# Kernel optimization log

Hardware: AMD Instinct MI355X
Metric: run time of the kernel (lower is better)

The kernel has to match this reference:

```python
import jax, jax.numpy as jnp
import numpy as np

S, V, H = 32, 16, 8            # hidden_scalars, hidden_vectors, num_heads
N, E = 10000, 100000           # nodes, edges
NRB, RH = 16, 64               # radial basis, radial MLP hidden
TH = S + 3 * V                 # packed irreps width (80)
WNUM = S * S + V * S + S * V + 2 * V * V  # TP weight_numel = 2560


def setup_inputs() -> dict:
    key = jax.random.key(0)
    ks = jax.random.split(key, 16)
    inp = {}
    inp["node_features"] = jax.random.normal(ks[0], (N, TH), jnp.float32)
    inp["edge_index"] = jax.random.randint(ks[1], (2, E), 0, N)
    inp["edge_sh"] = jax.random.normal(ks[2], (E, 4), jnp.float32)
    inp["edge_radial"] = jax.random.uniform(ks[3], (E, NRB), dtype=jnp.float32)
    inp["edge_envelope"] = jax.random.uniform(ks[4], (E,), dtype=jnp.float32)
    # radial MLP
    inp["W1"] = jax.random.normal(ks[5], (NRB, RH), jnp.float32) / np.sqrt(NRB)
    inp["b1"] = jnp.zeros((RH,), jnp.float32)
    inp["W2"] = jax.random.normal(ks[6], (RH, WNUM), jnp.float32) / np.sqrt(RH)
    inp["b2"] = jnp.zeros((WNUM,), jnp.float32)
    # attention query/key nets (scalar channels only)
    inp["Wq"] = jax.random.normal(ks[7], (S, H), jnp.float32) / np.sqrt(S)
    inp["bq"] = jnp.zeros((H,), jnp.float32)
    inp["Wk"] = jax.random.normal(ks[8], (S, H), jnp.float32) / np.sqrt(S)
    inp["bk"] = jnp.zeros((H,), jnp.float32)
    # equivariant linears (per-irrep channel mixing, e3nn style, no bias)
    inp["Wout_s"] = jax.random.normal(ks[9], (S, S), jnp.float32)
    inp["Wout_v"] = jax.random.normal(ks[10], (V, V), jnp.float32)
    inp["Wg_s"] = jax.random.normal(ks[11], (S, S + V), jnp.float32)
    inp["Wg_v"] = jax.random.normal(ks[12], (V, V), jnp.float32)
    # equivariant batch norm params
    inp["bn_ws"] = jnp.ones((S,), jnp.float32)
    inp["bn_bs"] = jnp.zeros((S,), jnp.float32)
    inp["bn_wv"] = jnp.ones((V,), jnp.float32)
    return inp


def _forward(node_features, edge_sh, edge_radial, edge_envelope,
             W1, b1, W2, b2, Wq, bq, Wk, bk,
             Wout_s, Wout_v, Wg_s, Wg_v, bn_ws, bn_bs, bn_wv, src, dst):
    # --- per-edge TP weights from radial MLP -> (E, WNUM), the big tensor ---
    tp_w = jax.nn.silu(edge_radial @ W1 + b1) @ W2 + b2
    offs = np.cumsum([0, S * S, V * S, S * V, V * V, V * V])
    WA = tp_w[:, offs[0]:offs[1]].reshape(-1, S, S)  # 0e x 0e -> 0e
    WB = tp_w[:, offs[1]:offs[2]].reshape(-1, V, S)  # 1o x 1o -> 0e
    WC = tp_w[:, offs[2]:offs[3]].reshape(-1, S, V)  # 0e x 1o -> 1o
    WD = tp_w[:, offs[3]:offs[4]].reshape(-1, V, V)  # 1o x 0e -> 1o
    WE = tp_w[:, offs[4]:offs[5]].reshape(-1, V, V)  # 1o x 1o -> 1o (cross)

    # --- gather source features, split irreps ---
    s_src = node_features[src, :S]                       # (E, S)
    v_src = node_features[src, S:].reshape(-1, V, 3)     # (E, V, 3)
    y0 = edge_sh[:, 0:1]                                 # (E, 1) l=0
    y1 = edge_sh[:, 1:4]                                 # (E, 3) l=1

    a0 = 1.0 / np.sqrt(S + V)       # path normalization, 0e output
    a1 = 1.0 / np.sqrt(S + 2 * V)   # path normalization, 1o output

    dot = (v_src * y1[:, None, :]).sum(-1) / np.sqrt(3.0)          # (E, V)
    msg_s = a0 * (jnp.einsum('es,esk->ek', s_src * y0, WA)
                  + jnp.einsum('ev,evk->ek', dot, WB))             # (E, S)
    crs = jnp.cross(v_src, y1[:, None, :]) / np.sqrt(2.0)          # (E, V, 3)
    msg_v = a1 * (jnp.einsum('es,ec,esk->ekc', s_src, y1, WC)
                  + jnp.einsum('evc,evk->ekc', v_src * y0[:, :, None], WD)
                  + jnp.einsum('evc,evk->ekc', crs, WE))           # (E, V, 3)
    messages = jnp.concatenate([msg_s, msg_v.reshape(-1, 3 * V)], axis=-1)

    # --- scatter-softmax attention over incoming edges per destination ---
    q = node_features[dst, :S] @ Wq + bq                 # (E, H)
    k = msg_s @ Wk + bk                                  # (E, H)
    logits = (q * k).sum(-1) / np.sqrt(H) + jnp.log(edge_envelope + 1e-8)
    mx = jax.ops.segment_max(logits, dst, num_segments=N)
    ex = jnp.exp(logits - mx[dst])
    den = jax.ops.segment_sum(ex, dst, num_segments=N)
    attn = ex / (den[dst] + 1e-8)                        # (E,)

    agg = jax.ops.segment_sum(attn[:, None] * messages, dst, num_segments=N)

    # --- equivariant output linear ---
    agg_s = agg[:, :S] @ Wout_s / np.sqrt(S)
    agg_v = jnp.einsum('nvc,vw->nwc', agg[:, S:].reshape(-1, V, 3), Wout_v) / np.sqrt(V)

    # --- gate ---
    gs = agg_s @ Wg_s / np.sqrt(S)                       # (N, S+V)
    gv = jnp.einsum('nvc,vw->nwc', agg_v, Wg_v) / np.sqrt(V)
    s = jax.nn.silu(gs[:, :S])
    g = jax.nn.sigmoid(gs[:, S:])
    v = g[:, :, None] * gv
    act = jnp.concatenate([s, v.reshape(-1, 3 * V)], axis=-1)

    # --- residual + equivariant batch norm ---
    x = act + node_features
    xs = x[:, :S]
    xv = x[:, S:].reshape(-1, V, 3)
    mean = xs.mean(0)
    var = xs.var(0)
    xs = (xs - mean) / jnp.sqrt(var + 1e-5) * bn_ws + bn_bs
    vn = (xv * xv).mean(-1).mean(0)                      # (V,) component norm
    xv = xv * (bn_wv / jnp.sqrt(vn + 1e-5))[None, :, None]
    return jnp.concatenate([xs, xv.reshape(-1, 3 * V)], axis=-1)


def reference(node_features, edge_index, edge_sh, edge_radial, edge_envelope,
              W1, b1, W2, b2, Wq, bq, Wk, bk,
              Wout_s, Wout_v, Wg_s, Wg_v, bn_ws, bn_bs, bn_wv):
    src, dst = edge_index[0], edge_index[1]
    return _forward(node_features, edge_sh, edge_radial, edge_envelope,
                    W1, b1, W2, b2, Wq, bq, Wk, bk,
                    Wout_s, Wout_v, Wg_s, Wg_v, bn_ws, bn_bs, bn_wv, src, dst)
```

## Files before the change

kernel.cpp:

```cpp
#include <hip/hip_runtime.h>
#include <math.h>

typedef __bf16 bf16x8 __attribute__((ext_vector_type(8)));
typedef __bf16 bf16x4 __attribute__((ext_vector_type(4)));
typedef float  f32x4  __attribute__((ext_vector_type(4)));
typedef float  f32x2  __attribute__((ext_vector_type(2)));
typedef unsigned long long u64x2 __attribute__((ext_vector_type(2)));

__device__ __forceinline__ float silu_f(float x){ return x / (1.f + __expf(-x)); }
__device__ __forceinline__ float sigm_f(float x){ return 1.f / (1.f + __expf(-x)); }

__device__ __forceinline__ float ntld_f(const float* p){
  return __builtin_nontemporal_load(p);
}
__device__ __forceinline__ float ntbf(const __bf16* p){
  unsigned short us = __builtin_nontemporal_load((const unsigned short*)p);
  union { unsigned u; float f; } cv; cv.u = ((unsigned)us) << 16;
  return cv.f;
}
__device__ __forceinline__ void nt_store_f(float* p, float v){
  __builtin_nontemporal_store(v, p);
}
__device__ __forceinline__ void nt_store_b8(__bf16* p, bf16x8 v){
  u64x2 u; __builtin_memcpy(&u, &v, 16);
  __builtin_nontemporal_store(u, (u64x2*)p);
}
__device__ __forceinline__ f32x2 b4lo(bf16x4 v){ f32x2 r; r[0]=(float)v[0]; r[1]=(float)v[1]; return r; }
__device__ __forceinline__ f32x2 b4hi(bf16x4 v){ f32x2 r; r[0]=(float)v[2]; r[1]=(float)v[3]; return r; }

__global__ void __launch_bounds__(256) k_setup(const float* __restrict__ W2,
    __bf16* __restrict__ W2t, const int* __restrict__ ei, int* __restrict__ cnt,
    const float* __restrict__ nf, const float* __restrict__ Wq,
    const float* __restrict__ bq, const float* __restrict__ Wk,
    const float* __restrict__ bk, float* __restrict__ kvt, float* __restrict__ carr,
    int nbPrep, int nbHist, int N, int E){
  int b = blockIdx.x, t = threadIdx.x;
  if (b < nbPrep){
    int gid = b*256 + t;
    int h = gid / 2560;
    int col = gid - h*2560;
    W2t[(size_t)(h>>5)*81920 + col*32 + (h&31)] = (__bf16)ntld_f(&W2[gid]);
    return;
  }
  if (b < nbPrep + nbHist){
    int e = (b - nbPrep)*256 + t;
    if (e < E) atomicAdd(&cnt[ei[E+e]], 1);
    return;
  }
  __shared__ float M[32][33];
  __shared__ float mb[32];
  __shared__ float nfl[64][33];
  __shared__ float bqbk_s;
  const int n0 = (b - nbPrep - nbHist)*64;
  for (int idx = t; idx < 1024; idx += 256){
    int s = idx >> 5, i = idx & 31;
    float acc = 0.f;
    #pragma unroll
    for (int j = 0; j < 8; ++j) acc += Wq[s*8+j]*Wk[i*8+j];
    M[s][i] = acc;
  }
  if (t < 32){
    float acc = 0.f;
    #pragma unroll
    for (int j = 0; j < 8; ++j) acc += Wq[t*8+j]*bk[j];
    mb[t] = acc;
  }
  if (t == 0){
    float acc = 0.f;
    #pragma unroll
    for (int j = 0; j < 8; ++j) acc += bq[j]*bk[j];
    bqbk_s = acc;
  }
  for (int idx = t; idx < 2048; idx += 256){
    int nl = idx >> 5, s = idx & 31;
    int n = n0 + nl;
    nfl[nl][s] = (n < N) ? nf[(size_t)n*80 + s] : 0.f;
  }
  __syncthreads();
  for (int idx = t; idx < 2048; idx += 256){
    int nl = idx >> 5, i = idx & 31;
    int n = n0 + nl;
    if (n < N){
      float acc = 0.f;
      #pragma unroll 8
      for (int s = 0; s < 32; ++s) acc += nfl[nl][s]*M[s][i];
      kvt[(size_t)n*32 + i] = acc;
    }
  }
  if (t < 64){
    int n = n0 + t;
    if (n < N){
      float acc = bqbk_s;
      #pragma unroll 8
      for (int s = 0; s < 32; ++s) acc += nfl[t][s]*mb[s];
      carr[n] = acc;
    }
  }
}

__global__ void __launch_bounds__(1024) k_scan(const int* __restrict__ cnt,
    int* __restrict__ cursor, float* __restrict__ bnacc, int N, int E){
  __shared__ int part[1024];
  int t = threadIdx.x;
  if (t < 80) bnacc[t] = 0.f;
  int chunk = (N + 1023) >> 10;
  int lo = t*chunk, hi = min(lo+chunk, N);
  int s = 0;
  for (int i = lo; i < hi; ++i) s += cnt[i];
  part[t] = s;
  __syncthreads();
  for (int off = 1; off < 1024; off <<= 1){
    int v = (t >= off) ? part[t-off] : 0;
    __syncthreads();
    part[t] += v;
    __syncthreads();
  }
  int base = (t == 0) ? 0 : part[t-1];
  for (int i = lo; i < hi; ++i){
    cursor[i] = base;
    base += cnt[i];
  }
}

__global__ void __launch_bounds__(256) k_prep(
    const float* __restrict__ nf, const int* __restrict__ ei,
    const float* __restrict__ sh, const float* __restrict__ radial,
    const float* __restrict__ W1, const float* __restrict__ b1,
    int* __restrict__ cursor,
    __bf16* __restrict__ uG, __bf16* __restrict__ cabG, __bf16* __restrict__ cvG,
    int* __restrict__ permG, int E, int NT)
{
  __shared__ float featT[80][65];
  __shared__ float radl[64][17];
  __shared__ float shlT[4][64];
  __shared__ float w1l[1024];
  __shared__ float b1l[64];
  __shared__ __align__(16) __bf16 u_l[64][72];
  __shared__ __align__(16) __bf16 cab_l[48][64];
  __shared__ __align__(16) __bf16 cv_l[64][3][64];
  __shared__ int src_l[64];

  const int t = threadIdx.x;
  const int e0 = blockIdx.x*64;
  const int tg0 = blockIdx.x*4;

  if (t < 64){
    int ee = e0 + t;
    if (ee < E){
      src_l[t] = ei[ee];
      permG[ee] = atomicAdd(&cursor[ei[(size_t)E+ee]], 1);
    } else src_l[t] = ei[E-1];
    b1l[t] = b1[t];
  }
  {
    int e = t >> 2, c = t & 3;
    int ec = min(e0+e, E-1);
    shlT[c][e] = ntld_f(&sh[(size_t)ec*4+c]);
  }
  for (int i = t; i < 1024; i += 256){
    int e = i >> 4, r = i & 15;
    int ec = min(e0+e, E-1);
    radl[e][r] = ntld_f(&radial[(size_t)ec*16+r]);
  }
  *(float4*)&w1l[t*4] = ((const float4*)W1)[t];
  __syncthreads();

  for (int i = t; i < 5120; i += 256){
    int e = i / 80, idx = i - e*80;
    featT[idx][e] = nf[(size_t)src_l[e]*80 + idx];
  }
  for (int i = t; i < 4096; i += 256){
    int e = i & 63, h = i >> 6;
    float acc = b1l[h];
    #pragma unroll
    for (int r = 0; r < 16; ++r) acc += radl[e][r]*w1l[r*64+h];
    u_l[e][h] = (__bf16)silu_f(acc);
  }
  __syncthreads();

  const float inv_s3 = 0.57735026918962576f;
  const float inv_s2 = 0.70710678118654752f;
  const float a0 = 0.14433756729740643f;
  const float a1 = 0.125f;

  for (int i = t; i < 3072; i += 256){
    int r = i >> 6, e = i & 63;
    float val;
    if (r < 32) val = a0 * shlT[0][e] * featT[r][e];
    else {
      int v = r - 32;
      float dot = (featT[32+v*3][e]*shlT[1][e] + featT[33+v*3][e]*shlT[2][e]
                 + featT[34+v*3][e]*shlT[3][e]) * inv_s3;
      val = a0 * dot;
    }
    cab_l[r][e] = (__bf16)val;
  }
  for (int i = t; i < 12288; i += 256){
    int e = i & 63, r = (i >> 6) & 63, c = i >> 12;
    float val;
    if (r < 32) val = a1 * shlT[1+c][e] * featT[r][e];
    else if (r < 48){
      int v = r - 32;
      val = a1 * shlT[0][e] * featT[32+v*3+c][e];
    } else {
      int v = r - 48;
      int c1 = c+1; if (c1 > 2) c1 -= 3;
      int c2 = c+2; if (c2 > 2) c2 -= 3;
      val = a1 * inv_s2 * (featT[32+v*3+c1][e]*shlT[1+c2][e]
                         - featT[32+v*3+c2][e]*shlT[1+c1][e]);
    }
    cv_l[r][c][e] = (__bf16)val;
  }
  __syncthreads();

  for (int i = t; i < 512; i += 256){
    int tl = i >> 7, rem = i & 127, k8 = rem >> 4, e = rem & 15;
    if (tg0 + tl < NT){
      bf16x8 v = *(const bf16x8*)&u_l[tl*16 + e][k8*8];
      *(bf16x8*)((char*)uG + (size_t)(tg0+tl)*2048 + k8*256 + e*16) = v;
    }
  }
  for (int i = t; i < 384; i += 256){
    int tl = i / 96, rem = i - tl*96, r = rem >> 1, h = rem & 1;
    if (tg0 + tl < NT){
      bf16x8 v = *(const bf16x8*)&cab_l[r][tl*16 + h*8];
      *(bf16x8*)((char*)cabG + (size_t)(tg0+tl)*1536 + r*32 + h*16) = v;
    }
  }
  for (int i = t; i < 1536; i += 256){
    int tl = i / 384, rem = i - tl*384, r = rem / 6, rem2 = rem - r*6,
        c = rem2 >> 1, h = rem2 & 1;
    if (tg0 + tl < NT){
      bf16x8 v = *(const bf16x8*)&cv_l[r][c][tl*16 + h*8];
      *(bf16x8*)((char*)cvG + (size_t)(tg0+tl)*6144 + r*96 + c*32 + h*16) = v;
    }
  }
}

#define LOAD_PANEL(BASE_IT, NITS) do {                                         \
    for (int idx = t; idx < (NITS)*128; idx += 512){                           \
      int itl_ = idx >> 7, rem_ = idx & 127, half_ = rem_ >> 6, r6_ = rem_ & 63;\
      int col_ = r6_ >> 2, quad_ = r6_ & 3;                                    \
      *(float4*)(panel + itl_*2048 + half_*1024 + quad_*256 + col_*16) =       \
        *(const float4*)(w2b + half_*163840 + (size_t)((BASE_IT)+itl_)*1024    \
                         + col_*64 + quad_*16);                                \
    }                                                                          \
    for (int i = t; i < (NITS)*16; i += 512) b2l[i] = b2[(BASE_IT)*16 + i];    \
  } while(0)

#define CAB_STAGE(TGC, BASE) do {                                              \
    bf16x8 x_ = *(const bf16x8*)(cabGb + (size_t)(TGC)*1536 + lane*16);        \
    bf16x4 y_ = *(const bf16x4*)(cabGb + (size_t)(TGC)*1536 + 1024 + lane*8);  \
    *(bf16x8*)(myCab + (BASE) + lane*16) = x_;                                 \
    *(bf16x4*)(myCab + (BASE) + 1024 + lane*8) = y_;                           \
  } while(0)

#define CV_STAGE(TGC, BASE, HALF) do {                                         \
    bf16x8 c0_ = *(const bf16x8*)(cvGb + (size_t)(TGC)*6144 + (HALF)*3072 + lane*48);\
    bf16x8 c1_ = *(const bf16x8*)(cvGb + (size_t)(TGC)*6144 + (HALF)*3072 + lane*48 + 16);\
    bf16x8 c2_ = *(const bf16x8*)(cvGb + (size_t)(TGC)*6144 + (HALF)*3072 + lane*48 + 32);\
    *(bf16x8*)(myCab + (BASE) + lane*48)      = c0_;                           \
    *(bf16x8*)(myCab + (BASE) + lane*48 + 16) = c1_;                           \
    *(bf16x8*)(myCab + (BASE) + lane*48 + 32) = c2_;                           \
  } while(0)

#define S_PAIR(SECOND, CBA, CBB, TA, TB) do {                                  \
    _Pragma("unroll 4")                                                        \
    for (int itl = 0; itl < 48; ++itl){                                        \
      bf16x8 B0_ = *(const bf16x8*)(panel + itl*2048 + laneOff);               \
      bf16x8 B1_ = *(const bf16x8*)(panel + itl*2048 + 1024 + laneOff);        \
      f32x4 dA_; dA_[0]=0;dA_[1]=0;dA_[2]=0;dA_[3]=0; f32x4 dB_ = dA_;         \
      dA_ = __builtin_amdgcn_mfma_f32_16x16x32_bf16(u##TA##_0, B0_, dA_, 0,0,0);\
      dB_ = __builtin_amdgcn_mfma_f32_16x16x32_bf16(u##TB##_0, B0_, dB_, 0,0,0);\
      dA_ = __builtin_amdgcn_mfma_f32_16x16x32_bf16(u##TA##_1, B1_, dA_, 0,0,0);\
      dB_ = __builtin_amdgcn_mfma_f32_16x16x32_bf16(u##TB##_1, B1_, dB_, 0,0,0);\
      const float bias_ = b2l[itl*16 + nlo];                                   \
      f32x2 bb_; bb_[0]=bias_; bb_[1]=bias_;                                   \
      f32x2 dAlo_ = __builtin_shufflevector(dA_,dA_,0,1) + bb_;                \
      f32x2 dAhi_ = __builtin_shufflevector(dA_,dA_,2,3) + bb_;                \
      f32x2 dBlo_ = __builtin_shufflevector(dB_,dB_,0,1) + bb_;                \
      f32x2 dBhi_ = __builtin_shufflevector(dB_,dB_,2,3) + bb_;                \
      const int r_ = (SECOND)*24 + (itl>>1);                                   \
      bf16x4 cA_ = *(const bf16x4*)(myCab + (CBA) + r_*32 + quad*8);           \
      bf16x4 cB_ = *(const bf16x4*)(myCab + (CBB) + r_*32 + quad*8);           \
      if (itl & 1){                                                            \
        s1l##TA += b4lo(cA_)*dAlo_; s1h##TA += b4hi(cA_)*dAhi_;                \
        s1l##TB += b4lo(cB_)*dBlo_; s1h##TB += b4hi(cB_)*dBhi_;                \
      } else {                                                                 \
        s0l##TA += b4lo(cA_)*dAlo_; s0h##TA += b4hi(cA_)*dAhi_;                \
        s0l##TB += b4lo(cB_)*dBlo_; s0h##TB += b4hi(cB_)*dBhi_;                \
      }                                                                        \
    }                                                                          \
  } while(0)

#define V_PAIR(TA, TB) do {                                                    \
    _Pragma("unroll 4")                                                        \
    for (int itl = 0; itl < 32; ++itl){                                        \
      bf16x8 B0_ = *(const bf16x8*)(panel + itl*2048 + laneOff);               \
      bf16x8 B1_ = *(const bf16x8*)(panel + itl*2048 + 1024 + laneOff);        \
      f32x4 dA_; dA_[0]=0;dA_[1]=0;dA_[2]=0;dA_[3]=0; f32x4 dB_ = dA_;         \
      dA_ = __builtin_amdgcn_mfma_f32_16x16x32_bf16(u##TA##_0, B0_, dA_, 0,0,0);\
      dB_ = __builtin_amdgcn_mfma_f32_16x16x32_bf16(u##TB##_0, B0_, dB_, 0,0,0);\
      dA_ = __builtin_amdgcn_mfma_f32_16x16x32_bf16(u##TA##_1, B1_, dA_, 0,0,0);\
      dB_ = __builtin_amdgcn_mfma_f32_16x16x32_bf16(u##TB##_1, B1_, dB_, 0,0,0);\
      const float bias_ = b2l[itl*16 + nlo];                                   \
      f32x2 bb_; bb_[0]=bias_; bb_[1]=bias_;                                   \
      f32x2 dAlo_ = __builtin_shufflevector(dA_,dA_,0,1) + bb_;                \
      f32x2 dAhi_ = __builtin_shufflevector(dA_,dA_,2,3) + bb_;                \
      f32x2 dBlo_ = __builtin_shufflevector(dB_,dB_,0,1) + bb_;                \
      f32x2 dBhi_ = __builtin_shufflevector(dB_,dB_,2,3) + bb_;                \
      const char* cbA_ = myCab + itl*96;                                       \
      const char* cbB_ = myCab + 3072 + itl*96;                                \
      bf16x4 q0_ = *(const bf16x4*)(cbA_ + quad*8);                            \
      bf16x4 q1_ = *(const bf16x4*)(cbA_ + 32 + quad*8);                       \
      bf16x4 q2_ = *(const bf16x4*)(cbA_ + 64 + quad*8);                       \
      v0l##TA += b4lo(q0_)*dAlo_; v0h##TA += b4hi(q0_)*dAhi_;                  \
      v1l##TA += b4lo(q1_)*dAlo_; v1h##TA += b4hi(q1_)*dAhi_;                  \
      v2l##TA += b4lo(q2_)*dAlo_; v2h##TA += b4hi(q2_)*dAhi_;                  \
      q0_ = *(const bf16x4*)(cbB_ + quad*8);                                   \
      q1_ = *(const bf16x4*)(cbB_ + 32 + quad*8);                              \
      q2_ = *(const bf16x4*)(cbB_ + 64 + quad*8);                              \
      v0l##TB += b4lo(q0_)*dBlo_; v0h##TB += b4hi(q0_)*dBhi_;                  \
      v1l##TB += b4lo(q1_)*dBlo_; v1h##TB += b4hi(q1_)*dBhi_;                  \
      v2l##TB += b4lo(q2_)*dBlo_; v2h##TB += b4hi(q2_)*dBhi_;                  \
    }                                                                          \
  } while(0)

#define S_FLUSH(TG, S0LO, S0HI, S1LO, S1HI) do {                               \
      myOut[(eb+0)*56 + nlo] = S0LO[0];                                        \
      myOut[(eb+1)*56 + nlo] = S0LO[1];                                        \
      myOut[(eb+2)*56 + nlo] = S0HI[0];                                        \
      myOut[(eb+3)*56 + nlo] = S0HI[1];                                        \
      myOut[(eb+0)*56 + 16+nlo] = S1LO[0];                                     \
      myOut[(eb+1)*56 + 16+nlo] = S1LO[1];                                     \
      myOut[(eb+2)*56 + 16+nlo] = S1HI[0];                                     \
      myOut[(eb+3)*56 + 16+nlo] = S1HI[1];                                     \
      const int e0e = (TG)*16;                                                 \
      { int e = lane>>2, seg = lane&3, eg = e0e + e;                           \
        if (eg < E){                                                           \
          f32x4 m0 = *(const f32x4*)&myOut[e*56 + seg*8];                      \
          f32x4 m1 = *(const f32x4*)&myOut[e*56 + seg*8 + 4];                  \
          bf16x8 o; o[0]=(__bf16)m0[0]; o[1]=(__bf16)m0[1];                    \
          o[2]=(__bf16)m0[2]; o[3]=(__bf16)m0[3]; o[4]=(__bf16)m1[0];          \
          o[5]=(__bf16)m1[1]; o[6]=(__bf16)m1[2]; o[7]=(__bf16)m1[3];          \
          nt_store_b8(msgs + (size_t)permG[eg]*80 + seg*8, o);                 \
        } }                                                                    \
      for (int r8 = 0; r8 < 2; ++r8){                                          \
        int e = r8*8 + (lane>>3), kq = lane&7, eg = e0e + e;                   \
        f32x4 ms = *(const f32x4*)&myOut[e*56 + kq*4];                         \
        int dn = ei[(size_t)E + min(eg, E-1)];                                 \
        const float* kvp = kvt + (size_t)dn*32 + kq*4;                         \
        float part = ms[0]*kvp[0]+ms[1]*kvp[1]+ms[2]*kvp[2]+ms[3]*kvp[3];      \
        part += __shfl_xor(part, 1);                                           \
        part += __shfl_xor(part, 2);                                           \
        part += __shfl_xor(part, 4);                                           \
        if (kq == 0 && eg < E){                                                \
          float lg = (part + carr[dn]) * 0.35355339059327373f                  \
                   + logf(ntld_f(&env[eg]) + 1e-8f);                           \
          nt_store_f(&logits_s[permG[eg]], lg);                                \
        } }                                                                    \
  } while(0)

#define V_FLUSH(TG, V0LO, V0HI, V1LO, V1HI, V2LO, V2HI) do {                   \
      const int cb2 = nlo*3;                                                   \
      myOut[(eb+0)*56 + cb2+0] = V0LO[0];                                      \
      myOut[(eb+1)*56 + cb2+0] = V0LO[1];                                      \
      myOut[(eb+2)*56 + cb2+0] = V0HI[0];                                      \
      myOut[(eb+3)*56 + cb2+0] = V0HI[1];                                      \
      myOut[(eb+0)*56 + cb2+1] = V1LO[0];                                      \
      myOut[(eb+1)*56 + cb2+1] = V1LO[1];                                      \
      myOut[(eb+2)*56 + cb2+1] = V1HI[0];                                      \
      myOut[(eb+3)*56 + cb2+1] = V1HI[1];                                      \
      myOut[(eb+0)*56 + cb2+2] = V2LO[0];                                      \
      myOut[(eb+1)*56 + cb2+2] = V2LO[1];                                      \
      myOut[(eb+2)*56 + cb2+2] = V2HI[0];                                      \
      myOut[(eb+3)*56 + cb2+2] = V2HI[1];                                      \
      const int e0e = (TG)*16;                                                 \
      for (int i = lane; i < 96; i += 64){                                     \
        int e = i/6, seg = i - (i/6)*6, eg = e0e + e;                          \
        if (eg < E){                                                           \
          f32x4 m0 = *(const f32x4*)&myOut[e*56 + seg*8];                      \
          f32x4 m1 = *(const f32x4*)&myOut[e*56 + seg*8 + 4];                  \
          bf16x8 o; o[0]=(__bf16)m0[0]; o[1]=(__bf16)m0[1];                    \
          o[2]=(__bf16)m0[2]; o[3]=(__bf16)m0[3]; o[4]=(__bf16)m1[0];          \
          o[5]=(__bf16)m1[1]; o[6]=(__bf16)m1[2]; o[7]=(__bf16)m1[3];          \
          nt_store_b8(msgs + (size_t)permG[eg]*80 + 32 + seg*8, o);            \
        } }                                                                    \
  } while(0)

__global__ void __launch_bounds__(512, 1) k_edge(
    const __bf16* __restrict__ W2t, const float* __restrict__ b2,
    const __bf16* __restrict__ uG, const __bf16* __restrict__ cabG,
    const __bf16* __restrict__ cvG, const int* __restrict__ ei,
    const int* __restrict__ permG, const float* __restrict__ kvt,
    const float* __restrict__ carr, const float* __restrict__ env,
    __bf16* __restrict__ msgs, float* __restrict__ logits_s, int E, int NT)
{
  __shared__ __align__(16) char panel[98304];
  __shared__ __align__(16) char wstage[8][6144];
  __shared__ float b2l[768];

  const int t = threadIdx.x;
  const int lane = t & 63;
  const int wv   = t >> 6;
  const int quad = lane >> 4;
  const int nlo  = lane & 15;
  const int wgid = blockIdx.x*8 + wv;
  const int laneOff = quad*256 + nlo*16;
  const int uOff    = quad*256 + nlo*16;
  char*  myCab = wstage[wv];
  float* myOut = (float*)wstage[wv];
  const char* w2b   = (const char*)W2t;
  const char* uGb   = (const char*)uG;
  const char* cabGb = (const char*)cabG;
  const char* cvGb  = (const char*)cvG;

  const int tA0 = wgid, tB0 = wgid + 2048, tA1 = wgid + 4096, tB1 = wgid + 6144;
  const bool hA0 = tA0 < NT, hB0 = tB0 < NT, hA1 = tA1 < NT, hB1 = tB1 < NT;
  const int cA0 = min(tA0, NT-1), cB0 = min(tB0, NT-1);
  const int cA1 = min(tA1, NT-1), cB1 = min(tB1, NT-1);

  const bf16x8 uA0_0 = *(const bf16x8*)(uGb + (size_t)cA0*2048 + uOff);
  const bf16x8 uA0_1 = *(const bf16x8*)(uGb + (size_t)cA0*2048 + 1024 + uOff);
  const bf16x8 uB0_0 = *(const bf16x8*)(uGb + (size_t)cB0*2048 + uOff);
  const bf16x8 uB0_1 = *(const bf16x8*)(uGb + (size_t)cB0*2048 + 1024 + uOff);
  const bf16x8 uA1_0 = *(const bf16x8*)(uGb + (size_t)cA1*2048 + uOff);
  const bf16x8 uA1_1 = *(const bf16x8*)(uGb + (size_t)cA1*2048 + 1024 + uOff);
  const bf16x8 uB1_0 = *(const bf16x8*)(uGb + (size_t)cB1*2048 + uOff);
  const bf16x8 uB1_1 = *(const bf16x8*)(uGb + (size_t)cB1*2048 + 1024 + uOff);

  f32x2 s0lA0={0,0}, s0hA0={0,0}, s1lA0={0,0}, s1hA0={0,0};
  f32x2 s0lB0={0,0}, s0hB0={0,0}, s1lB0={0,0}, s1hB0={0,0};
  f32x2 s0lA1={0,0}, s0hA1={0,0}, s1lA1={0,0}, s1hA1={0,0};
  f32x2 s0lB1={0,0}, s0hB1={0,0}, s1lB1={0,0}, s1hB1={0,0};

  const int eb = quad*4;

  LOAD_PANEL(0, 48);
  CAB_STAGE(cA0, 0); CAB_STAGE(cB0, 1536); CAB_STAGE(cA1, 3072); CAB_STAGE(cB1, 4608);
  __syncthreads();
  S_PAIR(0, 0, 1536, A0, B0);
  S_PAIR(0, 3072, 4608, A1, B1);
  __syncthreads();
  LOAD_PANEL(48, 48);
  __syncthreads();
  S_PAIR(1, 0, 1536, A0, B0);
  S_PAIR(1, 3072, 4608, A1, B1);
  if (hA0) S_FLUSH(tA0, s0lA0, s0hA0, s1lA0, s1hA0);
  if (hB0) S_FLUSH(tB0, s0lB0, s0hB0, s1lB0, s1hB0);
  if (hA1) S_FLUSH(tA1, s0lA1, s0hA1, s1lA1, s1hA1);
  if (hB1) S_FLUSH(tB1, s0lB1, s0hB1, s1lB1, s1hB1);
  __syncthreads();

  f32x2 v0lA0={0,0}, v0hA0={0,0}, v1lA0={0,0}, v1hA0={0,0}, v2lA0={0,0}, v2hA0={0,0};
  f32x2 v0lB0={0,0}, v0hB0={0,0}, v1lB0={0,0}, v1hB0={0,0}, v2lB0={0,0}, v2hB0={0,0};
  f32x2 v0lA1={0,0}, v0hA1={0,0}, v1lA1={0,0}, v1hA1={0,0}, v2lA1={0,0}, v2hA1={0,0};
  f32x2 v0lB1={0,0}, v0hB1={0,0}, v1lB1={0,0}, v1hB1={0,0}, v2lB1={0,0}, v2hB1={0,0};

  LOAD_PANEL(96, 32);
  CV_STAGE(cA0, 0, 0); CV_STAGE(cB0, 3072, 0);
  __syncthreads();
  V_PAIR(A0, B0);
  CV_STAGE(cA1, 0, 0); CV_STAGE(cB1, 3072, 0);
  V_PAIR(A1, B1);
  __syncthreads();
  LOAD_PANEL(128, 32);
  CV_STAGE(cA0, 0, 1); CV_STAGE(cB0, 3072, 1);
  __syncthreads();
  V_PAIR(A0, B0);
  CV_STAGE(cA1, 0, 1); CV_STAGE(cB1, 3072, 1);
  V_PAIR(A1, B1);
  if (hA0) V_FLUSH(tA0, v0lA0, v0hA0, v1lA0, v1hA0, v2lA0, v2hA0);
  if (hB0) V_FLUSH(tB0, v0lB0, v0hB0, v1lB0, v1hB0, v2lB0, v2hB0);
  if (hA1) V_FLUSH(tA1, v0lA1, v0hA1, v1lA1, v1hA1, v2lA1, v2hA1);
  if (hB1) V_FLUSH(tB1, v0lB1, v0hB1, v1lB1, v1hB1, v2lB1, v2hB1);
}

__global__ void __launch_bounds__(256) k_agg(
    const __bf16* __restrict__ msgs, const float* __restrict__ logits_s,
    const int* __restrict__ cursor, const float* __restrict__ nf,
    const float* __restrict__ Wout_s, const float* __restrict__ Wout_v,
    const float* __restrict__ Wg_s, const float* __restrict__ Wg_v,
    float* __restrict__ xbuf, float* __restrict__ bnacc, int N)
{
  __shared__ float aggl[4][80];
  __shared__ float t1[4][96];
  __shared__ float t2[4][96];
  __shared__ float bnl[80];
  const int t = threadIdx.x, l = t & 63, wv = t >> 6;
  const int n = blockIdx.x*4 + wv;
  const bool act = (n < N);
  const int nc = act ? n : (N-1);
  if (t < 80) bnl[t] = 0.f;

  const int r0 = (nc == 0) ? 0 : cursor[nc-1];
  const int r1 = cursor[nc];
  const int deg = act ? (r1 - r0) : 0;

  float mym = -3.4e38f;
  for (int i = l; i < deg; i += 64) mym = fmaxf(mym, logits_s[r0+i]);
  #pragma unroll
  for (int s = 32; s; s >>= 1) mym = fmaxf(mym, __shfl_xor(mym, s));
  float denp = 0.f, acc0 = 0.f, acc1 = 0.f;
  for (int c0 = 0; c0 < deg; c0 += 64){
    const int len = min(64, deg - c0);
    float ex = 0.f;
    if (l < len) ex = __expf(logits_s[r0+c0+l] - mym);
    denp += ex;
    for (int j0 = 0; j0 < len; j0 += 4){
      const int jn = len - j0;
      const __bf16* base = msgs + (size_t)(r0+c0+j0)*80;
      float v0=0,v1=0,v2=0,v3=0, w0=0,w1=0,w2=0,w3=0;
      float a0_=0,a1_=0,a2_=0,a3_=0;
      v0 = ntbf(&base[l]); if (l < 16) w0 = ntbf(&base[64+l]); a0_ = __shfl(ex, j0);
      if (jn > 1){ v1 = ntbf(&base[80+l]);  if (l < 16) w1 = ntbf(&base[144+l]); a1_ = __shfl(ex, j0+1); }
      if (jn > 2){ v2 = ntbf(&base[160+l]); if (l < 16) w2 = ntbf(&base[224+l]); a2_ = __shfl(ex, j0+2); }
      if (jn > 3){ v3 = ntbf(&base[240+l]); if (l < 16) w3 = ntbf(&base[304+l]); a3_ = __shfl(ex, j0+3); }
      acc0 += a0_*v0 + a1_*v1 + a2_*v2 + a3_*v3;
      if (l < 16) acc1 += a0_*w0 + a1_*w1 + a2_*w2 + a3_*w3;
    }
  }
  #pragma unroll
  for (int s = 32; s; s >>= 1) denp += __shfl_xor(denp, s);
  const float inv = 1.f/(denp + 1e-8f);
  aggl[wv][l] = acc0 * inv;
  if (l < 16) aggl[wv][64+l] = acc1 * inv;
  __syncthreads();

  const float* arow = &aggl[wv][0];
  const float iS = 0.17677669529663687f;
  const float iV = 0.25f;
  for (int o = l; o < 80; o += 64){
    float val = 0.f;
    if (o < 32){
      for (int s = 0; s < 32; ++s) val += arow[s]*Wout_s[s*32+o];
      val *= iS;
    } else {
      int w = (o-32)/3, c = (o-32)-w*3;
      for (int v = 0; v < 16; ++v) val += arow[32+v*3+c]*Wout_v[v*16+w];
      val *= iV;
    }
    t1[wv][o] = val;
  }
  __syncthreads();
  for (int o = l; o < 96; o += 64){
    float val = 0.f;
    if (o < 48){
      for (int k = 0; k < 32; ++k) val += t1[wv][k]*Wg_s[k*48+o];
      val *= iS;
    } else {
      int w = (o-48)/3, c = (o-48)-w*3;
      for (int v = 0; v < 16; ++v) val += t1[wv][32+v*3+c]*Wg_v[v*16+w];
      val *= iV;
    }
    t2[wv][o] = val;
  }
  __syncthreads();
  for (int o = l; o < 80; o += 64){
    float x;
    if (o < 32){
      x = silu_f(t2[wv][o]) + nf[(size_t)nc*80+o];
      if (act){
        nt_store_f(&xbuf[(size_t)n*80+o], x);
        atomicAdd(&bnl[o], x);
        atomicAdd(&bnl[32+o], x*x);
      }
    } else {
      int w = (o-32)/3;
      x = sigm_f(t2[wv][32+w]) * t2[wv][48+(o-32)] + nf[(size_t)nc*80+o];
      if (act){
        nt_store_f(&xbuf[(size_t)n*80+o], x);
        atomicAdd(&bnl[64+w], x*x);
      }
    }
  }
  __syncthreads();
  if (t < 80) atomicAdd(&bnacc[t], bnl[t]);
}

__global__ void __launch_bounds__(256) k_out(const float* __restrict__ xbuf,
    const float* __restrict__ bnacc,
    const float* __restrict__ bn_ws, const float* __restrict__ bn_bs,
    const float* __restrict__ bn_wv, float* __restrict__ out, int N){
  __shared__ float coef[80];
  int t = threadIdx.x;
  float fN = (float)N;
  if (t < 32){
    float mean = bnacc[t]/fN;
    float var = bnacc[32+t]/fN - mean*mean;
    float cm = bn_ws[t]*rsqrtf(var + 1e-5f);
    coef[t] = cm;
    coef[32+t] = bn_bs[t] - mean*cm;
  } else if (t < 48){
    int v = t - 32;
    coef[64+v] = bn_wv[v]*rsqrtf(bnacc[64+v]/(3.f*fN) + 1e-5f);
  }
  __syncthreads();
  int i = blockIdx.x*256 + t;
  if (i >= N*80) return;
  int o = i - (i/80)*80;
  float x = ntld_f(&xbuf[i]);
  nt_store_f(&out[i], (o < 32) ? (x*coef[o] + coef[32+o]) : (x*coef[64+(o-32)/3]));
}

extern "C" void kernel_launch(void* const* d_in, const int* in_sizes, int n_in,
                              void* d_out, int out_size, void* d_ws, size_t ws_size,
                              hipStream_t stream) {
  const float* nf     = (const float*)d_in[0];
  const int*   ei     = (const int*)  d_in[1];
  const float* sh     = (const float*)d_in[2];
  const float* radial = (const float*)d_in[3];
  const float* env    = (const float*)d_in[4];
  const float* W1     = (const float*)d_in[5];
  const float* b1     = (const float*)d_in[6];
  const float* W2     = (const float*)d_in[7];
  const float* b2     = (const float*)d_in[8];
  const float* Wq     = (const float*)d_in[9];
  const float* bq     = (const float*)d_in[10];
  const float* Wk     = (const float*)d_in[11];
  const float* bk     = (const float*)d_in[12];
  const float* Wout_s = (const float*)d_in[13];
  const float* Wout_v = (const float*)d_in[14];
  const float* Wg_s   = (const float*)d_in[15];
  const float* Wg_v   = (const float*)d_in[16];
  const float* bn_ws  = (const float*)d_in[17];
  const float* bn_bs  = (const float*)d_in[18];
  const float* bn_wv  = (const float*)d_in[19];

  const int E = in_sizes[4];
  const int N = in_sizes[0] / 80;
  const int NT = (E + 15)/16;

  float* ws = (float*)d_ws;
  size_t off = 0;
  __bf16* w2t    = (__bf16*)(ws + off); off += 81920;
  __bf16* msgs   = (__bf16*)(ws + off); off += (size_t)E*40;
  float* logits_s= ws + off; off += E;
  int* cnt       = (int*)(ws + off); off += N;
  int* cursor    = (int*)(ws + off); off += N;
  float* xbuf    = ws + off; off += (size_t)N*80;
  float* bnacc   = ws + off; off += 80;
  float* kvt     = ws + off; off += (size_t)N*32;
  float* carr    = ws + off; off += N;
  int* permG     = (int*)(ws + off); off += E;
  __bf16* uG     = (__bf16*)(ws + off); off += (size_t)NT*512;
  __bf16* cabG   = (__bf16*)(ws + off); off += (size_t)NT*384;
  __bf16* cvG    = (__bf16*)(ws + off); off += (size_t)NT*1536;

  hipMemsetAsync(cnt, 0, (size_t)N*sizeof(int), stream);

  const int nbPrep = 640;
  const int nbHist = (E + 255)/256;
  const int nbKv   = (N + 63)/64;
  k_setup<<<nbPrep + nbHist + nbKv, 256, 0, stream>>>(W2, w2t, ei, cnt,
      nf, Wq, bq, Wk, bk, kvt, carr, nbPrep, nbHist, N, E);
  k_scan<<<1, 1024, 0, stream>>>(cnt, cursor, bnacc, N, E);
  k_prep<<<(E + 63)/64, 256, 0, stream>>>(nf, ei, sh, radial, W1, b1, cursor,
      uG, cabG, cvG, permG, E, NT);
  k_edge<<<256, 512, 0, stream>>>(w2t, b2, uG, cabG, cvG, ei, permG,
      kvt, carr, env, msgs, logits_s, E, NT);
  k_agg<<<(N + 3)/4, 256, 0, stream>>>(msgs, logits_s, cursor, nf,
      Wout_s, Wout_v, Wg_s, Wg_v, xbuf, bnacc, N);
  k_out<<<(N*80 + 255)/256, 256, 0, stream>>>(xbuf, bnacc, bn_ws, bn_bs, bn_wv,
      (float*)d_out, N);
}
```

Measured before the change: 361.1 us.

## Double k_edge waves per block, halving per-wave tile count and staging buffers

```diff
diff --git a/kernel.cpp b/kernel.cpp
--- a/kernel.cpp
+++ b/kernel.cpp
@@ -238,14 +238,14 @@
 }
 
 #define LOAD_PANEL(BASE_IT, NITS) do {                                         \
-    for (int idx = t; idx < (NITS)*128; idx += 512){                           \
+    for (int idx = t; idx < (NITS)*128; idx += 1024){                          \
       int itl_ = idx >> 7, rem_ = idx & 127, half_ = rem_ >> 6, r6_ = rem_ & 63;\
       int col_ = r6_ >> 2, quad_ = r6_ & 3;                                    \
       *(float4*)(panel + itl_*2048 + half_*1024 + quad_*256 + col_*16) =       \
         *(const float4*)(w2b + half_*163840 + (size_t)((BASE_IT)+itl_)*1024    \
                          + col_*64 + quad_*16);                                \
     }                                                                          \
-    for (int i = t; i < (NITS)*16; i += 512) b2l[i] = b2[(BASE_IT)*16 + i];    \
+    for (int i = t; i < (NITS)*16; i += 1024) b2l[i] = b2[(BASE_IT)*16 + i];   \
   } while(0)
 
 #define CAB_STAGE(TGC, BASE) do {                                              \
@@ -255,13 +255,15 @@
     *(bf16x4*)(myCab + (BASE) + 1024 + lane*8) = y_;                           \
   } while(0)
 
-#define CV_STAGE(TGC, BASE, HALF) do {                                         \
-    bf16x8 c0_ = *(const bf16x8*)(cvGb + (size_t)(TGC)*6144 + (HALF)*3072 + lane*48);\
-    bf16x8 c1_ = *(const bf16x8*)(cvGb + (size_t)(TGC)*6144 + (HALF)*3072 + lane*48 + 16);\
-    bf16x8 c2_ = *(const bf16x8*)(cvGb + (size_t)(TGC)*6144 + (HALF)*3072 + lane*48 + 32);\
-    *(bf16x8*)(myCab + (BASE) + lane*48)      = c0_;                           \
-    *(bf16x8*)(myCab + (BASE) + lane*48 + 16) = c1_;                           \
-    *(bf16x8*)(myCab + (BASE) + lane*48 + 32) = c2_;                           \
+#define CV_STAGE_SUB(TGC, BASE, HALF, SUB) do {                                \
+    const char* s_ = cvGb + (size_t)(TGC)*6144 + (HALF)*3072 + (SUB)*1536      \
+                   + lane*24;                                                  \
+    bf16x4 a_ = *(const bf16x4*)(s_);                                          \
+    bf16x4 b_ = *(const bf16x4*)(s_ + 8);                                      \
+    bf16x4 c_ = *(const bf16x4*)(s_ + 16);                                     \
+    *(bf16x4*)(myCab + (BASE) + lane*24)      = a_;                            \
+    *(bf16x4*)(myCab + (BASE) + lane*24 + 8)  = b_;                            \
+    *(bf16x4*)(myCab + (BASE) + lane*24 + 16) = c_;                            \
   } while(0)
 
 #define S_PAIR(SECOND, CBA, CBB, TA, TB) do {                                  \
@@ -293,24 +295,25 @@
     }                                                                          \
   } while(0)
 
-#define V_PAIR(TA, TB) do {                                                    \
+#define V_PAIR_SUB(SUB, TA, TB) do {                                           \
     _Pragma("unroll 4")                                                        \
-    for (int itl = 0; itl < 32; ++itl){                                        \
-      bf16x8 B0_ = *(const bf16x8*)(panel + itl*2048 + laneOff);               \
-      bf16x8 B1_ = *(const bf16x8*)(panel + itl*2048 + 1024 + laneOff);        \
+    for (int il = 0; il < 16; ++il){                                           \
+      const int gitl = (SUB)*16 + il;                                          \
+      bf16x8 B0_ = *(const bf16x8*)(panel + gitl*2048 + laneOff);              \
+      bf16x8 B1_ = *(const bf16x8*)(panel + gitl*2048 + 1024 + laneOff);       \
       f32x4 dA_; dA_[0]=0;dA_[1]=0;dA_[2]=0;dA_[3]=0; f32x4 dB_ = dA_;         \
       dA_ = __builtin_amdgcn_mfma_f32_16x16x32_bf16(u##TA##_0, B0_, dA_, 0,0,0);\
       dB_ = __builtin_amdgcn_mfma_f32_16x16x32_bf16(u##TB##_0, B0_, dB_, 0,0,0);\
       dA_ = __builtin_amdgcn_mfma_f32_16x16x32_bf16(u##TA##_1, B1_, dA_, 0,0,0);\
       dB_ = __builtin_amdgcn_mfma_f32_16x16x32_bf16(u##TB##_1, B1_, dB_, 0,0,0);\
-      const float bias_ = b2l[itl*16 + nlo];                                   \
+      const float bias_ = b2l[gitl*16 + nlo];                                  \
       f32x2 bb_; bb_[0]=bias_; bb_[1]=bias_;                                   \
       f32x2 dAlo_ = __builtin_shufflevector(dA_,dA_,0,1) + bb_;                \
       f32x2 dAhi_ = __builtin_shufflevector(dA_,dA_,2,3) + bb_;                \
       f32x2 dBlo_ = __builtin_shufflevector(dB_,dB_,0,1) + bb_;                \
       f32x2 dBhi_ = __builtin_shufflevector(dB_,dB_,2,3) + bb_;                \
-      const char* cbA_ = myCab + itl*96;                                       \
-      const char* cbB_ = myCab + 3072 + itl*96;                                \
+      const char* cbA_ = myCab + il*96;                                        \
+      const char* cbB_ = myCab + 1536 + il*96;                                 \
       bf16x4 q0_ = *(const bf16x4*)(cbA_ + quad*8);                            \
       bf16x4 q1_ = *(const bf16x4*)(cbA_ + 32 + quad*8);                       \
       bf16x4 q2_ = *(const bf16x4*)(cbA_ + 64 + quad*8);                       \
@@ -388,7 +391,7 @@
         } }                                                                    \
   } while(0)
 
-__global__ void __launch_bounds__(512, 1) k_edge(
+__global__ void __launch_bounds__(1024, 4) k_edge(
     const __bf16* __restrict__ W2t, const float* __restrict__ b2,
     const __bf16* __restrict__ uG, const __bf16* __restrict__ cabG,
     const __bf16* __restrict__ cvG, const int* __restrict__ ei,
@@ -397,7 +400,7 @@
     __bf16* __restrict__ msgs, float* __restrict__ logits_s, int E, int NT)
 {
   __shared__ __align__(16) char panel[98304];
-  __shared__ __align__(16) char wstage[8][6144];
+  __shared__ __align__(16) char wstage[16][3584];
   __shared__ float b2l[768];
 
   const int t = threadIdx.x;
@@ -405,7 +408,7 @@
   const int wv   = t >> 6;
   const int quad = lane >> 4;
   const int nlo  = lane & 15;
-  const int wgid = blockIdx.x*8 + wv;
+  const int wgid = blockIdx.x*16 + wv;
   const int laneOff = quad*256 + nlo*16;
   const int uOff    = quad*256 + nlo*16;
   char*  myCab = wstage[wv];
@@ -415,65 +418,50 @@
   const char* cabGb = (const char*)cabG;
   const char* cvGb  = (const char*)cvG;
 
-  const int tA0 = wgid, tB0 = wgid + 2048, tA1 = wgid + 4096, tB1 = wgid + 6144;
-  const bool hA0 = tA0 < NT, hB0 = tB0 < NT, hA1 = tA1 < NT, hB1 = tB1 < NT;
-  const int cA0 = min(tA0, NT-1), cB0 = min(tB0, NT-1);
-  const int cA1 = min(tA1, NT-1), cB1 = min(tB1, NT-1);
-
-  const bf16x8 uA0_0 = *(const bf16x8*)(uGb + (size_t)cA0*2048 + uOff);
-  const bf16x8 uA0_1 = *(const bf16x8*)(uGb + (size_t)cA0*2048 + 1024 + uOff);
-  const bf16x8 uB0_0 = *(const bf16x8*)(uGb + (size_t)cB0*2048 + uOff);
-  const bf16x8 uB0_1 = *(const bf16x8*)(uGb + (size_t)cB0*2048 + 1024 + uOff);
-  const bf16x8 uA1_0 = *(const bf16x8*)(uGb + (size_t)cA1*2048 + uOff);
-  const bf16x8 uA1_1 = *(const bf16x8*)(uGb + (size_t)cA1*2048 + 1024 + uOff);
-  const bf16x8 uB1_0 = *(const bf16x8*)(uGb + (size_t)cB1*2048 + uOff);
-  const bf16x8 uB1_1 = *(const bf16x8*)(uGb + (size_t)cB1*2048 + 1024 + uOff);
-
-  f32x2 s0lA0={0,0}, s0hA0={0,0}, s1lA0={0,0}, s1hA0={0,0};
-  f32x2 s0lB0={0,0}, s0hB0={0,0}, s1lB0={0,0}, s1hB0={0,0};
-  f32x2 s0lA1={0,0}, s0hA1={0,0}, s1lA1={0,0}, s1hA1={0,0};
-  f32x2 s0lB1={0,0}, s0hB1={0,0}, s1lB1={0,0}, s1hB1={0,0};
+  const int tA = wgid, tB = wgid + 4096;
+  const bool hA = tA < NT, hB = tB < NT;
+  const int cA = min(tA, NT-1), cB = min(tB, NT-1);
+
+  const bf16x8 uA_0 = *(const bf16x8*)(uGb + (size_t)cA*2048 + uOff);
+  const bf16x8 uA_1 = *(const bf16x8*)(uGb + (size_t)cA*2048 + 1024 + uOff);
+  const bf16x8 uB_0 = *(const bf16x8*)(uGb + (size_t)cB*2048 + uOff);
+  const bf16x8 uB_1 = *(const bf16x8*)(uGb + (size_t)cB*2048 + 1024 + uOff);
+
+  f32x2 s0lA={0,0}, s0hA={0,0}, s1lA={0,0}, s1hA={0,0};
+  f32x2 s0lB={0,0}, s0hB={0,0}, s1lB={0,0}, s1hB={0,0};
 
   const int eb = quad*4;
 
   LOAD_PANEL(0, 48);
-  CAB_STAGE(cA0, 0); CAB_STAGE(cB0, 1536); CAB_STAGE(cA1, 3072); CAB_STAGE(cB1, 4608);
-  __syncthreads();
-  S_PAIR(0, 0, 1536, A0, B0);
-  S_PAIR(0, 3072, 4608, A1, B1);
+  CAB_STAGE(cA, 0); CAB_STAGE(cB, 1536);
+  __syncthreads();
+  S_PAIR(0, 0, 1536, A, B);
   __syncthreads();
   LOAD_PANEL(48, 48);
   __syncthreads();
-  S_PAIR(1, 0, 1536, A0, B0);
-  S_PAIR(1, 3072, 4608, A1, B1);
-  if (hA0) S_FLUSH(tA0, s0lA0, s0hA0, s1lA0, s1hA0);
-  if (hB0) S_FLUSH(tB0, s0lB0, s0hB0, s1lB0, s1hB0);
-  if (hA1) S_FLUSH(tA1, s0lA1, s0hA1, s1lA1, s1hA1);
-  if (hB1) S_FLUSH(tB1, s0lB1, s0hB1, s1lB1, s1hB1);
-  __syncthreads();
-
-  f32x2 v0lA0={0,0}, v0hA0={0,0}, v1lA0={0,0}, v1hA0={0,0}, v2lA0={0,0}, v2hA0={0,0};
-  f32x2 v0lB0={0,0}, v0hB0={0,0}, v1lB0={0,0}, v1hB0={0,0}, v2lB0={0,0}, v2hB0={0,0};
-  f32x2 v0lA1={0,0}, v0hA1={0,0}, v1lA1={0,0}, v1hA1={0,0}, v2lA1={0,0}, v2hA1={0,0};
-  f32x2 v0lB1={0,0}, v0hB1={0,0}, v1lB1={0,0}, v1hB1={0,0}, v2lB1={0,0}, v2hB1={0,0};
+  S_PAIR(1, 0, 1536, A, B);
+  if (hA) S_FLUSH(tA, s0lA, s0hA, s1lA, s1hA);
+  if (hB) S_FLUSH(tB, s0lB, s0hB, s1lB, s1hB);
+  __syncthreads();
+
+  f32x2 v0lA={0,0}, v0hA={0,0}, v1lA={0,0}, v1hA={0,0}, v2lA={0,0}, v2hA={0,0};
+  f32x2 v0lB={0,0}, v0hB={0,0}, v1lB={0,0}, v1hB={0,0}, v2lB={0,0}, v2hB={0,0};
 
   LOAD_PANEL(96, 32);
-  CV_STAGE(cA0, 0, 0); CV_STAGE(cB0, 3072, 0);
-  __syncthreads();
-  V_PAIR(A0, B0);
-  CV_STAGE(cA1, 0, 0); CV_STAGE(cB1, 3072, 0);
-  V_PAIR(A1, B1);
+  __syncthreads();
+  CV_STAGE_SUB(cA, 0, 0, 0); CV_STAGE_SUB(cB, 1536, 0, 0);
+  V_PAIR_SUB(0, A, B);
+  CV_STAGE_SUB(cA, 0, 0, 1); CV_STAGE_SUB(cB, 1536, 0, 1);
+  V_PAIR_SUB(1, A, B);
   __syncthreads();
   LOAD_PANEL(128, 32);
-  CV_STAGE(cA0, 0, 1); CV_STAGE(cB0, 3072, 1);
-  __syncthreads();
-  V_PAIR(A0, B0);
-  CV_STAGE(cA1, 0, 1); CV_STAGE(cB1, 3072, 1);
-  V_PAIR(A1, B1);
-  if (hA0) V_FLUSH(tA0, v0lA0, v0hA0, v1lA0, v1hA0, v2lA0, v2hA0);
-  if (hB0) V_FLUSH(tB0, v0lB0, v0hB0, v1lB0, v1hB0, v2lB0, v2hB0);
-  if (hA1) V_FLUSH(tA1, v0lA1, v0hA1, v1lA1, v1hA1, v2lA1, v2hA1);
-  if (hB1) V_FLUSH(tB1, v0lB1, v0hB1, v1lB1, v1hB1, v2lB1, v2hB1);
+  __syncthreads();
+  CV_STAGE_SUB(cA, 0, 1, 0); CV_STAGE_SUB(cB, 1536, 1, 0);
+  V_PAIR_SUB(0, A, B);
+  CV_STAGE_SUB(cA, 0, 1, 1); CV_STAGE_SUB(cB, 1536, 1, 1);
+  V_PAIR_SUB(1, A, B);
+  if (hA) V_FLUSH(tA, v0lA, v0hA, v1lA, v1hA, v2lA, v2hA);
+  if (hB) V_FLUSH(tB, v0lB, v0hB, v1lB, v1hB, v2lB, v2hB);
 }
 
 __global__ void __launch_bounds__(256) k_agg(
@@ -657,7 +645,7 @@
   k_scan<<<1, 1024, 0, stream>>>(cnt, cursor, bnacc, N, E);
   k_prep<<<(E + 63)/64, 256, 0, stream>>>(nf, ei, sh, radial, W1, b1, cursor,
       uG, cabG, cvG, permG, E, NT);
-  k_edge<<<256, 512, 0, stream>>>(w2t, b2, uG, cabG, cvG, ei, permG,
+  k_edge<<<256, 1024, 0, stream>>>(w2t, b2, uG, cabG, cvG, ei, permG,
       kvt, carr, env, msgs, logits_s, E, NT);
   k_agg<<<(N + 3)/4, 256, 0, stream>>>(msgs, logits_s, cursor, nf,
       Wout_s, Wout_v, Wg_s, Wg_v, xbuf, bnacc, N);
```

After: 355.5 us. About the same (-1.5%).
